# Optimization experiments

Measured on AMD Instinct MI355X. Metric: run time of the kernel, lower is better.

Reference implementation:

```python
import jax, jax.numpy as jnp
import numpy as np

NUM_CLASSES = 19
EPS_MEAN = 1e-6   # torch: denominator eps in per-class mean
EPS_COS = 1e-8    # torch CosineSimilarity default eps


def _nearest_resize_labels(target, H, W):
    # torch nn.Upsample(mode='nearest'): in_idx = floor(out_idx * in / out)
    th, tw = target.shape[1], target.shape[2]
    ih = (jnp.arange(H) * th) // H
    iw = (jnp.arange(W) * tw) // W
    return target[:, ih][:, :, iw]  # [B,H,W]


def _class_centers(feat, lab):
    # feat: [B,C,H,W]; lab: [B,H,W] int. Single-pass segment mean by class,
    # then scatter means back to pixels whose label is in [0, NUM_CLASSES).
    B, C, H, W = feat.shape
    f = feat.reshape(B, C, H * W)                 # [B,C,N]
    l = lab.reshape(B, H * W)                      # [B,N]
    onehot = jax.nn.one_hot(l, NUM_CLASSES, dtype=feat.dtype)  # [B,N,K]; out-of-range -> all-zero row
    sums = jnp.einsum('bcn,bnk->bck', f, onehot)   # per-class channel sums
    counts = onehot.sum(axis=1)                    # [B,K]
    means = sums / (counts[:, None, :] + EPS_MEAN) # [B,C,K]
    gathered = jnp.einsum('bck,bnk->bcn', means, onehot)  # mean at each valid pixel, 0 elsewhere
    valid = (l >= 0) & (l < NUM_CLASSES)           # [B,N]
    center = jnp.where(valid[:, None, :], gathered, f)
    return center.reshape(B, C, H, W)


def _cosine_dim1(a, b):
    # torch CosineSimilarity(dim=1): dot / (max(||a||,eps) * max(||b||,eps))
    num = (a * b).sum(axis=1)
    na = jnp.sqrt((a * a).sum(axis=1))
    nb = jnp.sqrt((b * b).sum(axis=1))
    return num / (jnp.maximum(na, EPS_COS) * jnp.maximum(nb, EPS_COS))


def setup_inputs() -> dict:
    key = jax.random.key(0)
    k1, k2, k3 = jax.random.split(key, 3)
    B, C, H, W = 8, 512, 64, 64
    preds_S = jax.random.normal(k1, (B, C, H, W), dtype=jnp.float32)
    preds_T = jax.random.normal(k2, (B, C, H, W), dtype=jnp.float32)
    target = jax.random.randint(k3, (B, 512, 512), 0, NUM_CLASSES, dtype=jnp.int64)
    return {"preds_S": preds_S, "preds_T": preds_T, "target": target}


def reference(preds_S, preds_T, target):
    H, W = preds_S.shape[2], preds_S.shape[3]
    lab = _nearest_resize_labels(target, H, W)     # [B,H,W]
    center_S = _class_centers(preds_S, lab)
    center_T = _class_centers(preds_T, lab)
    pcsim_S = _cosine_dim1(preds_S, center_S)      # [B,H,W]
    pcsim_T = _cosine_dim1(preds_T, center_T)
    return jnp.mean((pcsim_S - pcsim_T) ** 2)
```

## Files before the change

### kernel.cpp

```cpp
#include <hip/hip_runtime.h>

#define NCLS   19
#define NB     8
#define NC     512
#define NHW    4096
#define EPSM   1e-6f
#define EPSC   1e-8f

#define OFF_LABELS   0u
#define OFF_COUNTS   131072u
#define OFF_SUMS_S   132096u
#define OFF_SUMS_T   443392u
#define OFF_NORM_S   754688u
#define OFF_NORM_T   755712u

template<int CTRL>
__device__ __forceinline__ float dpp_add(float x) {
    int y = __builtin_amdgcn_update_dpp(0, __float_as_int(x), CTRL, 0xf, 0xf, false);
    return x + __int_as_float(y);
}
__device__ __forceinline__ float wave64_sum(float x) {
    x = dpp_add<0x111>(x);
    x = dpp_add<0x112>(x);
    x = dpp_add<0x114>(x);
    x = dpp_add<0x118>(x);
    x = dpp_add<0x142>(x);
    x = dpp_add<0x143>(x);
    return x;
}

__global__ __launch_bounds__(256) void k_labels(const int* __restrict__ target,
                                                int* __restrict__ labels,
                                                float* __restrict__ counts) {
    __shared__ int hist[NCLS];
    const int b = blockIdx.x;
    const int t = threadIdx.x;
    if (t < NCLS) hist[t] = 0;
    __syncthreads();
    const int* tb = target + (size_t)b * 512 * 512;
    #pragma unroll
    for (int i = 0; i < 16; ++i) {
        int n = t + i * 256;
        int y = n >> 6, x = n & 63;
        int l = tb[(y * 8) * 512 + x * 8];
        labels[b * NHW + n] = l;
        if (l >= 0 && l < NCLS) atomicAdd(&hist[l], 1);
    }
    __syncthreads();
    if (t < NCLS) counts[b * NCLS + t] = (float)hist[t];
}

__global__ __launch_bounds__(256) void k_sums(const float* __restrict__ fS,
                                              const float* __restrict__ fT,
                                              const int* __restrict__ labels,
                                              float* __restrict__ sumsS,
                                              float* __restrict__ sumsT) {
    __shared__ float2 acc[NCLS * 256];
    const int t   = threadIdx.x;
    const int blk = blockIdx.x;
    const int b   = blk >> 9;
    const int c   = blk & (NC - 1);

    const int4*   lab4 = (const int4*)(labels + b * NHW);
    const float4* pS   = (const float4*)(fS + ((size_t)(b * NC) + c) * NHW);
    const float4* pT   = (const float4*)(fT + ((size_t)(b * NC) + c) * NHW);

    int4 lab[4]; float4 vS[4]; float4 vT[4];
    #pragma unroll
    for (int j = 0; j < 4; ++j) {
        lab[j] = lab4[t + (j << 8)];
        vS[j]  = pS[t + (j << 8)];
        vT[j]  = pT[t + (j << 8)];
    }
    __builtin_amdgcn_sched_barrier(0);

    {
        float4* av = (float4*)acc;
        const float4 z = make_float4(0.f, 0.f, 0.f, 0.f);
        for (int i = t; i < NCLS * 128; i += 256) av[i] = z;
    }
    __syncthreads();

    float2* a0 = acc + t;

    #pragma unroll
    for (int j = 0; j < 4; ++j) {
        const int4   l = lab[j];
        const float4 s = vS[j];
        const float4 u = vT[j];
        if ((unsigned)l.x < NCLS) { float2 v = a0[l.x << 8]; v.x += s.x; v.y += u.x; a0[l.x << 8] = v; }
        if ((unsigned)l.y < NCLS) { float2 v = a0[l.y << 8]; v.x += s.y; v.y += u.y; a0[l.y << 8] = v; }
        if ((unsigned)l.z < NCLS) { float2 v = a0[l.z << 8]; v.x += s.z; v.y += u.z; a0[l.z << 8] = v; }
        if ((unsigned)l.w < NCLS) { float2 v = a0[l.w << 8]; v.x += s.w; v.y += u.w; a0[l.w << 8] = v; }
    }
    __syncthreads();

    const int w = t >> 6, lane = t & 63;
    for (int r = w; r < NCLS; r += 4) {
        const float2* row = acc + r * 256;
        const float2 p0 = row[lane], p1 = row[lane + 64];
        const float2 p2 = row[lane + 128], p3 = row[lane + 192];
        float sx = (p0.x + p1.x) + (p2.x + p3.x);
        float sy = (p0.y + p1.y) + (p2.y + p3.y);
        sx = wave64_sum(sx);
        sy = wave64_sum(sy);
        if (lane == 63) {
            sumsS[((size_t)(b * NCLS + r)) * NC + c] = sx;
            sumsT[((size_t)(b * NCLS + r)) * NC + c] = sy;
        }
    }
}

__global__ __launch_bounds__(64) void k_means(float* __restrict__ sumsS,
                                              float* __restrict__ sumsT,
                                              const float* __restrict__ counts,
                                              float* __restrict__ normS,
                                              float* __restrict__ normT,
                                              float* __restrict__ out) {
    const int bk = blockIdx.x;
    const int t = threadIdx.x;
    if (bk == 0 && t == 0) *out = 0.f;
    const float inv = 1.f / (counts[bk] + EPSM);
    float* rS = sumsS + (size_t)bk * NC;
    float* rT = sumsT + (size_t)bk * NC;
    float aS = 0.f, aT = 0.f;
    #pragma unroll
    for (int i = 0; i < NC / 64; ++i) {
        float mS = rS[t + i * 64] * inv; rS[t + i * 64] = mS; aS += mS * mS;
        float mT = rT[t + i * 64] * inv; rT[t + i * 64] = mT; aT += mT * mT;
    }
    aS = wave64_sum(aS);
    aT = wave64_sum(aT);
    if (t == 63) { normS[bk] = sqrtf(aS); normT[bk] = sqrtf(aT); }
}

__global__ __launch_bounds__(256) void k_dots(const float* __restrict__ fS,
                                              const float* __restrict__ fT,
                                              const float* __restrict__ meansS,
                                              const float* __restrict__ meansT,
                                              const int* __restrict__ labels,
                                              const float* __restrict__ normS,
                                              const float* __restrict__ normT,
                                              float* __restrict__ out) {
    __shared__ float2 mST[4 * NCLS * 65];
    __shared__ float4 red[4 * 64];
    const int t    = threadIdx.x;
    const int w    = t >> 6, px = t & 63;
    const int blk  = blockIdx.x;
    const int b    = blk >> 6;
    const int tile = blk & 63;
    const int n    = tile * 64 + px;

    const int l  = labels[b * NHW + n];
    const int lc = (l >= 0 && l < NCLS) ? l : 0;

    float dS = 0.f, nS = 0.f, dT = 0.f, nT = 0.f;
    #pragma unroll
    for (int r = 0; r < 2; ++r) {
        __syncthreads();
        for (int i = t; i < 4 * NCLS * 64; i += 256) {
            const int ww  = i / (NCLS * 64);
            const int rem = i - ww * (NCLS * 64);
            const int k   = rem >> 6, ci = rem & 63;
            const int c   = ww * 128 + r * 64 + ci;
            mST[(ww * NCLS + k) * 65 + ci] = make_float2(
                meansS[((size_t)(b * NCLS + k)) * NC + c],
                meansT[((size_t)(b * NCLS + k)) * NC + c]);
        }
        __syncthreads();
        const size_t base = ((size_t)(b * NC) + w * 128 + r * 64) * NHW + tile * 64 + px;
        const float* pS = fS + base;
        const float* pT = fT + base;
        const float2* m0 = mST + (w * NCLS + lc) * 65;
        #pragma unroll 8
        for (int ci = 0; ci < 64; ++ci) {
            const float vS = pS[(size_t)ci * NHW];
            const float vT = pT[(size_t)ci * NHW];
            const float2 m = m0[ci];
            dS += vS * m.x; nS += vS * vS;
            dT += vT * m.y; nT += vT * vT;
        }
    }
    red[w * 64 + px] = make_float4(dS, nS, dT, nT);
    __syncthreads();

    if (w == 0) {
        const float4 a0 = red[px],       a1 = red[64 + px];
        const float4 a2 = red[128 + px], a3 = red[192 + px];
        const float DS = (a0.x + a1.x) + (a2.x + a3.x);
        const float NS = (a0.y + a1.y) + (a2.y + a3.y);
        const float DT = (a0.z + a1.z) + (a2.z + a3.z);
        const float NT = (a0.w + a1.w) + (a2.w + a3.w);
        float val = 0.f;
        if (l >= 0 && l < NCLS) {
            const float cS = DS / (fmaxf(sqrtf(NS), EPSC) * fmaxf(normS[b * NCLS + l], EPSC));
            const float cT = DT / (fmaxf(sqrtf(NT), EPSC) * fmaxf(normT[b * NCLS + l], EPSC));
            const float d = cS - cT;
            val = d * d;
        }
        val = wave64_sum(val);
        if (px == 63) atomicAdd(out, val * (1.f / (NB * NHW)));
    }
}

extern "C" void kernel_launch(void* const* d_in, const int* in_sizes, int n_in,
                              void* d_out, int out_size, void* d_ws, size_t ws_size,
                              hipStream_t stream) {
    (void)in_sizes; (void)n_in; (void)out_size; (void)ws_size;
    const float* fS     = (const float*)d_in[0];
    const float* fT     = (const float*)d_in[1];
    const int*   target = (const int*)d_in[2];

    char* ws = (char*)d_ws;
    int*   labels = (int*)  (ws + OFF_LABELS);
    float* counts = (float*)(ws + OFF_COUNTS);
    float* sumsS  = (float*)(ws + OFF_SUMS_S);
    float* sumsT  = (float*)(ws + OFF_SUMS_T);
    float* normS  = (float*)(ws + OFF_NORM_S);
    float* normT  = (float*)(ws + OFF_NORM_T);

    k_labels<<<NB, 256, 0, stream>>>(target, labels, counts);
    k_sums  <<<NB * NC, 256, 0, stream>>>(fS, fT, labels, sumsS, sumsT);
    k_means <<<NB * NCLS, 64, 0, stream>>>(sumsS, sumsT, counts, normS, normT,
                                           (float*)d_out);
    k_dots  <<<NB * 64, 256, 0, stream>>>(fS, fT, sumsS, sumsT, labels,
                                          normS, normT, (float*)d_out);
}
```

Measured before the change: 194.8 us.

## Parallelize label downsampling and stage feature loads via direct global-to-LDS

Splits the label/histogram kernel across 8 blocks per batch, writing partial counts that k_means sums. This removes a serial, low-parallelism launch. In k_sums, the feature loads use global_load_lds into shared buffers instead of registers, then are read back for the class accumulation. The extra 32KB of LDS per block may reduce occupancy, and correctness relies on the barrier waiting for the LDS DMA writes.

```diff
diff --git a/kernel.cpp b/kernel.cpp
--- a/kernel.cpp
+++ b/kernel.cpp
@@ -6,13 +6,14 @@
 #define NHW    4096
 #define EPSM   1e-6f
 #define EPSC   1e-8f
+#define LBLK   8
 
 #define OFF_LABELS   0u
-#define OFF_COUNTS   131072u
 #define OFF_SUMS_S   132096u
 #define OFF_SUMS_T   443392u
 #define OFF_NORM_S   754688u
 #define OFF_NORM_T   755712u
+#define OFF_COUNTSP  756736u
 
 template<int CTRL>
 __device__ __forceinline__ float dpp_add(float x) {
@@ -29,25 +30,33 @@
     return x;
 }
 
+__device__ __forceinline__ void g2lds16(const float* g, float* l) {
+    __builtin_amdgcn_global_load_lds(
+        (const __attribute__((address_space(1))) float*)g,
+        (__attribute__((address_space(3))) float*)l, 16, 0, 0);
+}
+
 __global__ __launch_bounds__(256) void k_labels(const int* __restrict__ target,
                                                 int* __restrict__ labels,
-                                                float* __restrict__ counts) {
+                                                float* __restrict__ countsP) {
     __shared__ int hist[NCLS];
-    const int b = blockIdx.x;
+    const int blk  = blockIdx.x;
+    const int b    = blk >> 3;
+    const int part = blk & (LBLK - 1);
     const int t = threadIdx.x;
     if (t < NCLS) hist[t] = 0;
     __syncthreads();
     const int* tb = target + (size_t)b * 512 * 512;
     #pragma unroll
-    for (int i = 0; i < 16; ++i) {
-        int n = t + i * 256;
+    for (int i = 0; i < 2; ++i) {
+        int n = part * 512 + t + i * 256;
         int y = n >> 6, x = n & 63;
         int l = tb[(y * 8) * 512 + x * 8];
         labels[b * NHW + n] = l;
         if (l >= 0 && l < NCLS) atomicAdd(&hist[l], 1);
     }
     __syncthreads();
-    if (t < NCLS) counts[b * NCLS + t] = (float)hist[t];
+    if (t < NCLS) countsP[(size_t)blk * NCLS + t] = (float)hist[t];
 }
 
 __global__ __launch_bounds__(256) void k_sums(const float* __restrict__ fS,
@@ -56,23 +65,29 @@
                                               float* __restrict__ sumsS,
                                               float* __restrict__ sumsT) {
     __shared__ float2 acc[NCLS * 256];
+    __shared__ float  sA[NHW];
+    __shared__ float  sB[NHW];
     const int t   = threadIdx.x;
+    const int w   = t >> 6, lane = t & 63;
     const int blk = blockIdx.x;
     const int b   = blk >> 9;
     const int c   = blk & (NC - 1);
 
-    const int4*   lab4 = (const int4*)(labels + b * NHW);
-    const float4* pS   = (const float4*)(fS + ((size_t)(b * NC) + c) * NHW);
-    const float4* pT   = (const float4*)(fT + ((size_t)(b * NC) + c) * NHW);
-
-    int4 lab[4]; float4 vS[4]; float4 vT[4];
+    const size_t fbase = ((size_t)(b * NC) + c) * NHW;
+    const float* gS = fS + fbase + (w << 10) + (lane << 2);
+    const float* gT = fT + fbase + (w << 10) + (lane << 2);
+    float* lS = sA + (w << 10);
+    float* lT = sB + (w << 10);
     #pragma unroll
     for (int j = 0; j < 4; ++j) {
-        lab[j] = lab4[t + (j << 8)];
-        vS[j]  = pS[t + (j << 8)];
-        vT[j]  = pT[t + (j << 8)];
-    }
-    __builtin_amdgcn_sched_barrier(0);
+        g2lds16(gS + (j << 8), lS + (j << 8));
+        g2lds16(gT + (j << 8), lT + (j << 8));
+    }
+
+    const int4* lab4 = (const int4*)(labels + b * NHW);
+    int4 lab[4];
+    #pragma unroll
+    for (int j = 0; j < 4; ++j) lab[j] = lab4[t + (j << 8)];
 
     {
         float4* av = (float4*)acc;
@@ -84,10 +99,10 @@
     float2* a0 = acc + t;
 
     #pragma unroll
-    for (int j = 0; j < 4; ++j) {
-        const int4   l = lab[j];
-        const float4 s = vS[j];
-        const float4 u = vT[j];
+    for (int i = 0; i < 4; ++i) {
+        const float4 s = *(const float4*)(sA + (t << 2) + (i << 10));
+        const float4 u = *(const float4*)(sB + (t << 2) + (i << 10));
+        const int4   l = lab[i];
         if ((unsigned)l.x < NCLS) { float2 v = a0[l.x << 8]; v.x += s.x; v.y += u.x; a0[l.x << 8] = v; }
         if ((unsigned)l.y < NCLS) { float2 v = a0[l.y << 8]; v.x += s.y; v.y += u.y; a0[l.y << 8] = v; }
         if ((unsigned)l.z < NCLS) { float2 v = a0[l.z << 8]; v.x += s.z; v.y += u.z; a0[l.z << 8] = v; }
@@ -95,7 +110,6 @@
     }
     __syncthreads();
 
-    const int w = t >> 6, lane = t & 63;
     for (int r = w; r < NCLS; r += 4) {
         const float2* row = acc + r * 256;
         const float2 p0 = row[lane], p1 = row[lane + 64];
@@ -113,14 +127,18 @@
 
 __global__ __launch_bounds__(64) void k_means(float* __restrict__ sumsS,
                                               float* __restrict__ sumsT,
-                                              const float* __restrict__ counts,
+                                              const float* __restrict__ countsP,
                                               float* __restrict__ normS,
                                               float* __restrict__ normT,
                                               float* __restrict__ out) {
     const int bk = blockIdx.x;
     const int t = threadIdx.x;
     if (bk == 0 && t == 0) *out = 0.f;
-    const float inv = 1.f / (counts[bk] + EPSM);
+    const int b = bk / NCLS, k = bk - b * NCLS;
+    float cnt = 0.f;
+    #pragma unroll
+    for (int p = 0; p < LBLK; ++p) cnt += countsP[(size_t)(b * LBLK + p) * NCLS + k];
+    const float inv = 1.f / (cnt + EPSM);
     float* rS = sumsS + (size_t)bk * NC;
     float* rT = sumsT + (size_t)bk * NC;
     float aS = 0.f, aT = 0.f;
@@ -212,16 +230,16 @@
     const int*   target = (const int*)d_in[2];
 
     char* ws = (char*)d_ws;
-    int*   labels = (int*)  (ws + OFF_LABELS);
-    float* counts = (float*)(ws + OFF_COUNTS);
-    float* sumsS  = (float*)(ws + OFF_SUMS_S);
-    float* sumsT  = (float*)(ws + OFF_SUMS_T);
-    float* normS  = (float*)(ws + OFF_NORM_S);
-    float* normT  = (float*)(ws + OFF_NORM_T);
-
-    k_labels<<<NB, 256, 0, stream>>>(target, labels, counts);
+    int*   labels  = (int*)  (ws + OFF_LABELS);
+    float* sumsS   = (float*)(ws + OFF_SUMS_S);
+    float* sumsT   = (float*)(ws + OFF_SUMS_T);
+    float* normS   = (float*)(ws + OFF_NORM_S);
+    float* normT   = (float*)(ws + OFF_NORM_T);
+    float* countsP = (float*)(ws + OFF_COUNTSP);
+
+    k_labels<<<NB * LBLK, 256, 0, stream>>>(target, labels, countsP);
     k_sums  <<<NB * NC, 256, 0, stream>>>(fS, fT, labels, sumsS, sumsT);
-    k_means <<<NB * NCLS, 64, 0, stream>>>(sumsS, sumsT, counts, normS, normT,
+    k_means <<<NB * NCLS, 64, 0, stream>>>(sumsS, sumsT, countsP, normS, normT,
                                            (float*)d_out);
     k_dots  <<<NB * 64, 256, 0, stream>>>(fS, fT, sumsS, sumsT, labels,
                                           normS, normT, (float*)d_out);
```

Measured after the change: 190.3 us. 1.02x faster.
